# Optimization experiments

Hardware: AMD Instinct MI355X
Metric: run time of the kernel (lower is better)

Reference implementation:

```python
import jax, jax.numpy as jnp
import numpy as np

B, S, E, H = 2, 2048, 1024, 16
D = E // H  # head dim = 64


def setup_inputs() -> dict:
    key = jax.random.key(0)
    ks = jax.random.split(key, 6)
    x = jax.random.normal(ks[0], (B, S, E), dtype=jnp.float32)
    attn_mask = jax.random.bernoulli(ks[1], 0.1, (B, S, S))  # True = masked
    scale = 1.0 / np.sqrt(E)
    w_kernel = jax.random.normal(ks[2], (E, 3 * E), dtype=jnp.float32) * scale
    w_bias = jax.random.normal(ks[3], (3 * E,), dtype=jnp.float32) * 0.02
    fc_kernel = jax.random.normal(ks[4], (E, E), dtype=jnp.float32) * scale
    fc_bias = jax.random.normal(ks[5], (E,), dtype=jnp.float32) * 0.02
    return {"x": x, "attn_mask": attn_mask, "w_kernel": w_kernel,
            "w_bias": w_bias, "fc_kernel": fc_kernel, "fc_bias": fc_bias}


def reference(x, attn_mask, w_kernel, w_bias, fc_kernel, fc_bias):
    b, s, e = x.shape
    qkv = jnp.einsum("bse,ef->bsf", x, w_kernel) + w_bias  # (B,S,3E)
    q, k, v = jnp.split(qkv, 3, axis=-1)

    def heads(t):  # (B,S,E) -> (B,H,S,D)
        return t.reshape(b, s, H, D).transpose(0, 2, 1, 3)

    q, k, v = heads(q), heads(k), heads(v)
    scores = jnp.einsum("bhqd,bhkd->bhqk", q, k) / jnp.sqrt(jnp.float32(D))
    # faithful quirk: masked positions are filled with 1e-9, not -inf
    scores = jnp.where(attn_mask[:, None, :, :], jnp.float32(1e-9), scores)
    A = jax.nn.softmax(scores, axis=-1)
    out = jnp.einsum("bhqk,bhkd->bhqd", A, v)  # (B,H,S,D)
    out = out.transpose(0, 2, 1, 3).reshape(b, s, e)
    # dropout is identity in eval mode
    return jnp.einsum("bse,ef->bsf", out, fc_kernel) + fc_bias
```

## Files before the change

kernel.cpp:

```cpp
#include <hip/hip_runtime.h>
#include <math.h>

#define BB 2
#define SS 2048
#define EE 1024
#define HH 16

typedef _Float16 f16;
typedef __attribute__((ext_vector_type(8))) _Float16 f16x8;
typedef __attribute__((ext_vector_type(4))) _Float16 f16x4;
typedef __attribute__((ext_vector_type(2))) _Float16 f16x2;
typedef __attribute__((ext_vector_type(4))) float f32x4;

union P8 { f16x8 v8; f16x2 h2[4]; };
union V8 { f16x8 v8; f16x4 v4[2]; };

#define QSCALE 0.18033688011112042f

#if __has_builtin(__builtin_amdgcn_exp2f)
#define EXP2(x) __builtin_amdgcn_exp2f(x)
#else
#define EXP2(x) exp2f(x)
#endif

static __device__ __forceinline__ f16x2 pk2(float a, float b) {
#if __has_builtin(__builtin_amdgcn_cvt_pkrtz)
  return __builtin_bit_cast(f16x2, __builtin_amdgcn_cvt_pkrtz(a, b));
#else
  f16x2 r; r[0] = (f16)a; r[1] = (f16)b; return r;
#endif
}

static __device__ __forceinline__ void gl16(const void* g, void* l) {
  __builtin_amdgcn_global_load_lds(
      (const __attribute__((address_space(1))) void*)g,
      (__attribute__((address_space(3))) void*)l, 16, 0, 0);
}

__global__ __launch_bounds__(256) void cvt_f32_f16(
    const float* __restrict__ in, f16* __restrict__ out, int n)
{
  int i = (blockIdx.x * 256 + threadIdx.x) * 8;
  if (i >= n) return;
  float4 a = *(const float4*)(in + i);
  float4 b = *(const float4*)(in + i + 4);
  f16x8 o;
  o[0] = (f16)a.x; o[1] = (f16)a.y; o[2] = (f16)a.z; o[3] = (f16)a.w;
  o[4] = (f16)b.x; o[5] = (f16)b.y; o[6] = (f16)b.z; o[7] = (f16)b.w;
  *(f16x8*)(out + i) = o;
}

__global__ __launch_bounds__(256) void transpose_cvt(
    const float* __restrict__ in, f16* __restrict__ out, int K, int N)
{
  __shared__ float T[64][65];
  const int k0 = blockIdx.y * 64, n0 = blockIdx.x * 64;
  const int tr = threadIdx.x >> 4, tc = (threadIdx.x & 15) * 4;
#pragma unroll
  for (int i = 0; i < 4; ++i) {
    int r = tr + i * 16;
    *(float4*)&T[r][tc] = *(const float4*)(in + (size_t)(k0 + r) * N + n0 + tc);
  }
  __syncthreads();
#pragma unroll
  for (int i = 0; i < 4; ++i) {
    int nl = tr + i * 16;
    f16x4 v;
    v[0] = (f16)T[tc + 0][nl];
    v[1] = (f16)T[tc + 1][nl];
    v[2] = (f16)T[tc + 2][nl];
    v[3] = (f16)T[tc + 3][nl];
    *(f16x4*)(out + (size_t)(n0 + nl) * K + k0 + tc) = v;
  }
}

__global__ __launch_bounds__(256) void pack_mask(
    const int* __restrict__ m, unsigned long long* __restrict__ bits)
{
  const int i = blockIdx.x * 256 + threadIdx.x;
  const unsigned long long bal = __ballot(m[i] != 0);
  if ((threadIdx.x & 63) == 0) bits[i >> 6] = bal;
}

__global__ __launch_bounds__(256) void gemm_f16(
    const f16* __restrict__ A, const f16* __restrict__ Bt,
    const float* __restrict__ bias, int M, int N, int K, int mode,
    f16* __restrict__ oQK, f16* __restrict__ oVT, float* __restrict__ oF32)
{
  __shared__ f16 Ah[128 * 32];
  __shared__ f16 Bh[128 * 32];

  const int t = threadIdx.x;
  const int l = t & 63, w = t >> 6;
  const int l15 = l & 15, l4 = l >> 4;
  const int wr = w >> 1, wc = w & 1;
  const int n0 = blockIdx.x * 128, m0 = blockIdx.y * 128;

  const int srow = l >> 2;
  const int gch  = (l & 3) ^ (srow & 3);
  const f16* Ap0 = A + (size_t)(m0 + w * 32 + srow) * K + gch * 8;
  const f16* Ap1 = Ap0 + (size_t)16 * K;
  const f16* Bp0 = Bt + (size_t)(n0 + w * 32 + srow) * K + gch * 8;
  const f16* Bp1 = Bp0 + (size_t)16 * K;
  f16* ldsA0 = &Ah[(w * 32) * 32];
  f16* ldsA1 = &Ah[(w * 32 + 16) * 32];
  f16* ldsB0 = &Bh[(w * 32) * 32];
  f16* ldsB1 = &Bh[(w * 32 + 16) * 32];

  f32x4 acc[4][4] = {};
  const int csw = (l15 & 3);

  for (int k0 = 0; k0 < K; k0 += 32) {
    gl16(Ap0 + k0, ldsA0);
    gl16(Ap1 + k0, ldsA1);
    gl16(Bp0 + k0, ldsB0);
    gl16(Bp1 + k0, ldsB1);
    __syncthreads();

    f16x8 af[4], bf[4];
#pragma unroll
    for (int mr = 0; mr < 4; ++mr) {
      const int row = wr * 64 + mr * 16 + l15;
      af[mr] = *(const f16x8*)&Ah[row * 32 + ((l4 ^ csw) * 8)];
    }
#pragma unroll
    for (int nr = 0; nr < 4; ++nr) {
      const int row = wc * 64 + nr * 16 + l15;
      bf[nr] = *(const f16x8*)&Bh[row * 32 + ((l4 ^ csw) * 8)];
    }
#pragma unroll
    for (int mr = 0; mr < 4; ++mr)
#pragma unroll
      for (int nr = 0; nr < 4; ++nr)
        acc[mr][nr] = __builtin_amdgcn_mfma_f32_16x16x32_f16(
            af[mr], bf[nr], acc[mr][nr], 0, 0, 0);
    __syncthreads();
  }

  if (mode == 1) {
#pragma unroll
    for (int nr = 0; nr < 4; ++nr) {
      const int n = n0 + wc * 64 + nr * 16 + l15;
      const float bv = bias[n];
#pragma unroll
      for (int mr = 0; mr < 4; ++mr)
#pragma unroll
        for (int j = 0; j < 4; ++j) {
          const int m = m0 + wr * 64 + mr * 16 + l4 * 4 + j;
          oF32[(size_t)m * N + n] = acc[mr][nr][j] + bv;
        }
    }
  } else {
#pragma unroll
    for (int nr = 0; nr < 4; ++nr) {
      const int n = n0 + wc * 64 + nr * 16 + l15;
      const float bv = bias[n];
      if (n < 2048) {
        const float qs = (n < 1024) ? QSCALE : 1.0f;
#pragma unroll
        for (int mr = 0; mr < 4; ++mr)
#pragma unroll
          for (int j = 0; j < 4; ++j) {
            const int m = m0 + wr * 64 + mr * 16 + l4 * 4 + j;
            oQK[(size_t)m * 2048 + n] = (f16)((acc[mr][nr][j] + bv) * qs);
          }
      } else {
        const int hh = (n - 2048) >> 6;
        const int d = (n - 2048) & 63;
#pragma unroll
        for (int mr = 0; mr < 4; ++mr) {
          const int tok0 = m0 + wr * 64 + mr * 16 + l4 * 4;
          const int bq = tok0 >> 11, sq = tok0 & 2047;
          f16x4 v;
          v[0] = (f16)(acc[mr][nr][0] + bv);
          v[1] = (f16)(acc[mr][nr][1] + bv);
          v[2] = (f16)(acc[mr][nr][2] + bv);
          v[3] = (f16)(acc[mr][nr][3] + bv);
          *(f16x4*)(oVT + ((size_t)(bq * 16 + hh) * 64 + d) * SS + sq) = v;
        }
      }
    }
  }
}

__global__ __launch_bounds__(256, 2) void attn_mfma(
    const f16* __restrict__ qkbuf, const f16* __restrict__ vT,
    const unsigned long long* __restrict__ mbits, f16* __restrict__ aout)
{
  __shared__ f16 Kds[2][64 * 64];
  __shared__ f16 Vds[2][64 * 64];

  const int t = threadIdx.x;
  const int w = t >> 6, l = t & 63, l15 = l & 15, l4 = l >> 4;
  const int bh = blockIdx.y, b = bh >> 4, h = bh & 15;
  const int qbase = blockIdx.x * 128 + w * 32;

  f16x8 q00, q01, q10, q11;
  {
    const size_t r0 = (size_t)(b * SS + qbase + l15) * 2048 + h * 64;
    const size_t r1 = (size_t)(b * SS + qbase + 16 + l15) * 2048 + h * 64;
    q00 = *(const f16x8*)(qkbuf + r0 + l4 * 8);
    q01 = *(const f16x8*)(qkbuf + r0 + 32 + l4 * 8);
    q10 = *(const f16x8*)(qkbuf + r1 + l4 * 8);
    q11 = *(const f16x8*)(qkbuf + r1 + 32 + l4 * 8);
  }

  f32x4 accA[4] = {}, accB[4] = {};
  f32x4 accLA = {}, accLB = {};
  f16x8 ones;
#pragma unroll
  for (int i = 0; i < 8; ++i) ones[i] = (f16)1.0f;

  const unsigned long long* mA = mbits + (size_t)(b * SS + qbase + l15) * 32;
  const unsigned long long* mB = mbits + (size_t)(b * SS + qbase + 16 + l15) * 32;

  const int srow = t >> 3;
  const int scb  = (t & 7) * 8;
  const int sws  = (srow & 7) << 3;
  const f16* kb = qkbuf + (size_t)b * SS * 2048 + 1024 + h * 64 + scb;
  const f16* vb = vT + ((size_t)bh * 64 + srow) * SS + scb;

  f16x8 kr0, kr1, vr0, vr1;
#define LOADT(kt)                                                         \
  {                                                                       \
    kr0 = *(const f16x8*)(kb + (size_t)((kt) + srow) * 2048);             \
    kr1 = *(const f16x8*)(kb + (size_t)((kt) + srow + 32) * 2048);        \
    vr0 = *(const f16x8*)(vb + (kt));                                     \
    vr1 = *(const f16x8*)(vb + 32 * SS + (kt));                           \
  }
#define COMMIT(bi)                                                        \
  {                                                                       \
    *(f16x8*)&Kds[bi][srow * 64 + (scb ^ sws)]        = kr0;              \
    *(f16x8*)&Kds[bi][(srow + 32) * 64 + (scb ^ sws)] = kr1;              \
    *(f16x8*)&Vds[bi][srow * 64 + (scb ^ sws)]        = vr0;              \
    *(f16x8*)&Vds[bi][(srow + 32) * 64 + (scb ^ sws)] = vr1;              \
  }

  LOADT(0)
  COMMIT(0)
  LOADT(64)
  __syncthreads();

  const int swr = (l15 & 7) << 3;

  unsigned long long mbA = mA[0], mbB = mB[0];

  for (int tI = 0; tI < 32; ++tI) {
    const int cur = tI & 1;
    unsigned long long nmbA = 0, nmbB = 0;
    if (tI + 1 < 32) { nmbA = mA[tI + 1]; nmbB = mB[tI + 1]; }

#pragma unroll
    for (int sg = 0; sg < 2; ++sg) {
      float pA[8], pB[8];
#pragma unroll
      for (int gh = 0; gh < 2; ++gh) {
        const int g = sg * 2 + gh;
        const f16* krow = &Kds[cur][(g * 16 + l15) * 64];
        const f16x8 k0 = *(const f16x8*)(krow + ((l4 * 8) ^ swr));
        const f16x8 k1 = *(const f16x8*)(krow + ((32 + l4 * 8) ^ swr));
        f32x4 SA = __builtin_amdgcn_mfma_f32_16x16x32_f16(
            k0, q00, (f32x4){0.f, 0.f, 0.f, 0.f}, 0, 0, 0);
        SA = __builtin_amdgcn_mfma_f32_16x16x32_f16(k1, q01, SA, 0, 0, 0);
        f32x4 SB = __builtin_amdgcn_mfma_f32_16x16x32_f16(
            k0, q10, (f32x4){0.f, 0.f, 0.f, 0.f}, 0, 0, 0);
        SB = __builtin_amdgcn_mfma_f32_16x16x32_f16(k1, q11, SB, 0, 0, 0);

        const unsigned int nibA = (unsigned int)(mbA >> (g * 16 + l4 * 4));
        const unsigned int nibB = (unsigned int)(mbB >> (g * 16 + l4 * 4));
#pragma unroll
        for (int j = 0; j < 4; ++j) {
          pA[gh * 4 + j] = ((nibA >> j) & 1u) ? 1.0f : EXP2(SA[j]);
          pB[gh * 4 + j] = ((nibB >> j) & 1u) ? 1.0f : EXP2(SB[j]);
        }
      }
      P8 uA, uB;
      uA.h2[0] = pk2(pA[0], pA[1]); uA.h2[1] = pk2(pA[2], pA[3]);
      uA.h2[2] = pk2(pA[4], pA[5]); uA.h2[3] = pk2(pA[6], pA[7]);
      uB.h2[0] = pk2(pB[0], pB[1]); uB.h2[1] = pk2(pB[2], pB[3]);
      uB.h2[2] = pk2(pB[4], pB[5]); uB.h2[3] = pk2(pB[6], pB[7]);

#pragma unroll
      for (int dg = 0; dg < 4; ++dg) {
        const f16* vrow = &Vds[cur][(dg * 16 + l15) * 64];
        V8 uv;
        uv.v4[0] = *(const f16x4*)(vrow + ((sg * 32 + l4 * 4) ^ swr));
        uv.v4[1] = *(const f16x4*)(vrow + ((sg * 32 + 16 + l4 * 4) ^ swr));
        accA[dg] = __builtin_amdgcn_mfma_f32_16x16x32_f16(uA.v8, uv.v8, accA[dg], 0, 0, 0);
        accB[dg] = __builtin_amdgcn_mfma_f32_16x16x32_f16(uB.v8, uv.v8, accB[dg], 0, 0, 0);
      }
      accLA = __builtin_amdgcn_mfma_f32_16x16x32_f16(uA.v8, ones, accLA, 0, 0, 0);
      accLB = __builtin_amdgcn_mfma_f32_16x16x32_f16(uB.v8, ones, accLB, 0, 0, 0);
    }

    if (tI + 1 < 32) {
      COMMIT(cur ^ 1)
      if (tI + 2 < 32) LOADT((tI + 2) * 64)
    }
    __syncthreads();
    mbA = nmbA; mbB = nmbB;
  }

#pragma unroll
  for (int j = 0; j < 4; ++j) {
    const int qr = l4 * 4 + j;
    const float invA = 1.0f / accLA[j];
    const float invB = 1.0f / accLB[j];
    const size_t rowA = (size_t)(b * SS + qbase + qr) * EE + h * 64 + l15;
    const size_t rowB = (size_t)(b * SS + qbase + 16 + qr) * EE + h * 64 + l15;
#pragma unroll
    for (int dg = 0; dg < 4; ++dg) {
      aout[rowA + dg * 16] = (f16)(accA[dg][j] * invA);
      aout[rowB + dg * 16] = (f16)(accB[dg][j] * invB);
    }
  }
}

extern "C" void kernel_launch(void* const* d_in, const int* in_sizes, int n_in,
                              void* d_out, int out_size, void* d_ws,
                              size_t ws_size, hipStream_t stream)
{
  (void)in_sizes; (void)n_in; (void)out_size; (void)ws_size;
  const float* x   = (const float*)d_in[0];
  const int* mask  = (const int*)d_in[1];
  const float* wk  = (const float*)d_in[2];
  const float* wb  = (const float*)d_in[3];
  const float* fck = (const float*)d_in[4];
  const float* fcb = (const float*)d_in[5];
  float* out       = (float*)d_out;

  char* ws = (char*)d_ws;
  size_t off = 0;
  f16* xh    = (f16*)(ws + off); off += (size_t)4096 * 1024 * 2;
  f16* Wt    = (f16*)(ws + off); off += (size_t)3072 * 1024 * 2;
  f16* fckT  = (f16*)(ws + off); off += (size_t)1024 * 1024 * 2;
  f16* qk    = (f16*)(ws + off); off += (size_t)4096 * 2048 * 2;
  f16* vT    = (f16*)(ws + off); off += (size_t)BB * HH * 64 * SS * 2;
  f16* aoutH = (f16*)(ws + off); off += (size_t)4096 * 1024 * 2;
  unsigned long long* mbits = (unsigned long long*)(ws + off);
  off += (size_t)BB * SS * SS / 8;

  cvt_f32_f16<<<4096 * 1024 / (8 * 256), 256, 0, stream>>>(x, xh, 4096 * 1024);
  transpose_cvt<<<dim3(3072 / 64, 1024 / 64), 256, 0, stream>>>(wk, Wt, 1024, 3072);
  transpose_cvt<<<dim3(1024 / 64, 1024 / 64), 256, 0, stream>>>(fck, fckT, 1024, 1024);
  pack_mask<<<BB * SS * SS / 256, 256, 0, stream>>>(mask, mbits);

  gemm_f16<<<dim3(3072 / 128, 4096 / 128), 256, 0, stream>>>(
      xh, Wt, wb, 4096, 3072, 1024, 0, qk, vT, nullptr);

  attn_mfma<<<dim3(SS / 128, BB * HH), 256, 0, stream>>>(qk, vT, mbits, aoutH);

  gemm_f16<<<dim3(1024 / 128, 4096 / 128), 256, 0, stream>>>(
      aoutH, fckT, fcb, 4096, 1024, 1024, 1, nullptr, nullptr, out);
}
```

Measured before the change: 240.2 us.

## Split attention over two key halves, combine partials; add MFMA priority hints

The attention kernel gains a third grid dimension that splits the 2048 keys into two halves. Each block writes unnormalized fp16 partial outputs plus row sums, and a new combine kernel adds the two halves and normalizes them. The aim is twice as many blocks, for better CU occupancy and latency hiding. In exchange it adds a combine pass, extra global traffic for the partials, and fp16 rounding of the unnormalized partial sums. The change also wraps MFMA sections in s_setprio in both the GEMM and attention kernels, manually unrolls the tile loop by two, and reuses workspace memory for the partial buffers.

After: 253.6 us. 1.06x slower.

```diff
diff --git a/kernel.cpp b/kernel.cpp
--- a/kernel.cpp
+++ b/kernel.cpp
@@ -128,12 +128,14 @@
       const int row = wc * 64 + nr * 16 + l15;
       bf[nr] = *(const f16x8*)&Bh[row * 32 + ((l4 ^ csw) * 8)];
     }
+    __builtin_amdgcn_s_setprio(1);
 #pragma unroll
     for (int mr = 0; mr < 4; ++mr)
 #pragma unroll
       for (int nr = 0; nr < 4; ++nr)
         acc[mr][nr] = __builtin_amdgcn_mfma_f32_16x16x32_f16(
             af[mr], bf[nr], acc[mr][nr], 0, 0, 0);
+    __builtin_amdgcn_s_setprio(0);
     __syncthreads();
   }
 
@@ -185,7 +187,8 @@
 
 __global__ __launch_bounds__(256, 2) void attn_mfma(
     const f16* __restrict__ qkbuf, const f16* __restrict__ vT,
-    const unsigned long long* __restrict__ mbits, f16* __restrict__ aout)
+    const unsigned long long* __restrict__ mbits,
+    f16* __restrict__ Opart, float* __restrict__ Lpart)
 {
   __shared__ f16 Kds[2][64 * 64];
   __shared__ f16 Vds[2][64 * 64];
@@ -193,6 +196,7 @@
   const int t = threadIdx.x;
   const int w = t >> 6, l = t & 63, l15 = l & 15, l4 = l >> 4;
   const int bh = blockIdx.y, b = bh >> 4, h = bh & 15;
+  const int ks = blockIdx.z;
   const int qbase = blockIdx.x * 128 + w * 32;
 
   f16x8 q00, q01, q10, q11;
@@ -211,14 +215,17 @@
 #pragma unroll
   for (int i = 0; i < 8; ++i) ones[i] = (f16)1.0f;
 
-  const unsigned long long* mA = mbits + (size_t)(b * SS + qbase + l15) * 32;
-  const unsigned long long* mB = mbits + (size_t)(b * SS + qbase + 16 + l15) * 32;
+  const unsigned long long* mA =
+      mbits + (size_t)(b * SS + qbase + l15) * 32 + ks * 16;
+  const unsigned long long* mB =
+      mbits + (size_t)(b * SS + qbase + 16 + l15) * 32 + ks * 16;
 
   const int srow = t >> 3;
   const int scb  = (t & 7) * 8;
   const int sws  = (srow & 7) << 3;
-  const f16* kb = qkbuf + (size_t)b * SS * 2048 + 1024 + h * 64 + scb;
-  const f16* vb = vT + ((size_t)bh * 64 + srow) * SS + scb;
+  const f16* kb = qkbuf + (size_t)b * SS * 2048 + 1024 + h * 64 + scb +
+                  (size_t)ks * 1024 * 2048;
+  const f16* vb = vT + ((size_t)bh * 64 + srow) * SS + scb + ks * 1024;
 
   f16x8 kr0, kr1, vr0, vr1;
 #define LOADT(kt)                                                         \
@@ -243,77 +250,107 @@
 
   const int swr = (l15 & 7) << 3;
 
-  unsigned long long mbA = mA[0], mbB = mB[0];
-
-  for (int tI = 0; tI < 32; ++tI) {
-    const int cur = tI & 1;
-    unsigned long long nmbA = 0, nmbB = 0;
-    if (tI + 1 < 32) { nmbA = mA[tI + 1]; nmbB = mB[tI + 1]; }
-
-#pragma unroll
-    for (int sg = 0; sg < 2; ++sg) {
-      float pA[8], pB[8];
-#pragma unroll
-      for (int gh = 0; gh < 2; ++gh) {
-        const int g = sg * 2 + gh;
-        const f16* krow = &Kds[cur][(g * 16 + l15) * 64];
-        const f16x8 k0 = *(const f16x8*)(krow + ((l4 * 8) ^ swr));
-        const f16x8 k1 = *(const f16x8*)(krow + ((32 + l4 * 8) ^ swr));
-        f32x4 SA = __builtin_amdgcn_mfma_f32_16x16x32_f16(
-            k0, q00, (f32x4){0.f, 0.f, 0.f, 0.f}, 0, 0, 0);
-        SA = __builtin_amdgcn_mfma_f32_16x16x32_f16(k1, q01, SA, 0, 0, 0);
-        f32x4 SB = __builtin_amdgcn_mfma_f32_16x16x32_f16(
-            k0, q10, (f32x4){0.f, 0.f, 0.f, 0.f}, 0, 0, 0);
-        SB = __builtin_amdgcn_mfma_f32_16x16x32_f16(k1, q11, SB, 0, 0, 0);
-
-        const unsigned int nibA = (unsigned int)(mbA >> (g * 16 + l4 * 4));
-        const unsigned int nibB = (unsigned int)(mbB >> (g * 16 + l4 * 4));
-#pragma unroll
-        for (int j = 0; j < 4; ++j) {
-          pA[gh * 4 + j] = ((nibA >> j) & 1u) ? 1.0f : EXP2(SA[j]);
-          pB[gh * 4 + j] = ((nibB >> j) & 1u) ? 1.0f : EXP2(SB[j]);
-        }
-      }
-      P8 uA, uB;
-      uA.h2[0] = pk2(pA[0], pA[1]); uA.h2[1] = pk2(pA[2], pA[3]);
-      uA.h2[2] = pk2(pA[4], pA[5]); uA.h2[3] = pk2(pA[6], pA[7]);
-      uB.h2[0] = pk2(pB[0], pB[1]); uB.h2[1] = pk2(pB[2], pB[3]);
-      uB.h2[2] = pk2(pB[4], pB[5]); uB.h2[3] = pk2(pB[6], pB[7]);
-
-#pragma unroll
-      for (int dg = 0; dg < 4; ++dg) {
-        const f16* vrow = &Vds[cur][(dg * 16 + l15) * 64];
-        V8 uv;
-        uv.v4[0] = *(const f16x4*)(vrow + ((sg * 32 + l4 * 4) ^ swr));
-        uv.v4[1] = *(const f16x4*)(vrow + ((sg * 32 + 16 + l4 * 4) ^ swr));
-        accA[dg] = __builtin_amdgcn_mfma_f32_16x16x32_f16(uA.v8, uv.v8, accA[dg], 0, 0, 0);
-        accB[dg] = __builtin_amdgcn_mfma_f32_16x16x32_f16(uB.v8, uv.v8, accB[dg], 0, 0, 0);
-      }
-      accLA = __builtin_amdgcn_mfma_f32_16x16x32_f16(uA.v8, ones, accLA, 0, 0, 0);
-      accLB = __builtin_amdgcn_mfma_f32_16x16x32_f16(uB.v8, ones, accLB, 0, 0, 0);
-    }
-
-    if (tI + 1 < 32) {
-      COMMIT(cur ^ 1)
-      if (tI + 2 < 32) LOADT((tI + 2) * 64)
-    }
-    __syncthreads();
-    mbA = nmbA; mbB = nmbB;
-  }
-
+#define BODY(cur, tI)                                                         \
+  {                                                                           \
+    const unsigned long long mbA = mA[tI];                                    \
+    const unsigned long long mbB = mB[tI];                                    \
+    _Pragma("unroll")                                                         \
+    for (int sg = 0; sg < 2; ++sg) {                                          \
+      float pA[8], pB[8];                                                     \
+      _Pragma("unroll")                                                       \
+      for (int gh = 0; gh < 2; ++gh) {                                        \
+        const int g = sg * 2 + gh;                                            \
+        const f16* krow = &Kds[cur][(g * 16 + l15) * 64];                     \
+        const f16x8 k0 = *(const f16x8*)(krow + ((l4 * 8) ^ swr));            \
+        const f16x8 k1 = *(const f16x8*)(krow + ((32 + l4 * 8) ^ swr));       \
+        __builtin_amdgcn_s_setprio(1);                                        \
+        f32x4 SA = __builtin_amdgcn_mfma_f32_16x16x32_f16(                    \
+            k0, q00, (f32x4){0.f, 0.f, 0.f, 0.f}, 0, 0, 0);                   \
+        SA = __builtin_amdgcn_mfma_f32_16x16x32_f16(k1, q01, SA, 0, 0, 0);    \
+        f32x4 SB = __builtin_amdgcn_mfma_f32_16x16x32_f16(                    \
+            k0, q10, (f32x4){0.f, 0.f, 0.f, 0.f}, 0, 0, 0);                   \
+        SB = __builtin_amdgcn_mfma_f32_16x16x32_f16(k1, q11, SB, 0, 0, 0);    \
+        __builtin_amdgcn_s_setprio(0);                                        \
+        const unsigned int nibA = (unsigned int)(mbA >> (g * 16 + l4 * 4));   \
+        const unsigned int nibB = (unsigned int)(mbB >> (g * 16 + l4 * 4));   \
+        _Pragma("unroll")                                                     \
+        for (int j = 0; j < 4; ++j) {                                         \
+          pA[gh * 4 + j] = ((nibA >> j) & 1u) ? 1.0f : EXP2(SA[j]);           \
+          pB[gh * 4 + j] = ((nibB >> j) & 1u) ? 1.0f : EXP2(SB[j]);           \
+        }                                                                     \
+      }                                                                       \
+      P8 uA, uB;                                                              \
+      uA.h2[0] = pk2(pA[0], pA[1]); uA.h2[1] = pk2(pA[2], pA[3]);             \
+      uA.h2[2] = pk2(pA[4], pA[5]); uA.h2[3] = pk2(pA[6], pA[7]);             \
+      uB.h2[0] = pk2(pB[0], pB[1]); uB.h2[1] = pk2(pB[2], pB[3]);             \
+      uB.h2[2] = pk2(pB[4], pB[5]); uB.h2[3] = pk2(pB[6], pB[7]);             \
+      __builtin_amdgcn_s_setprio(1);                                          \
+      _Pragma("unroll")                                                       \
+      for (int dg = 0; dg < 4; ++dg) {                                        \
+        const f16* vrow = &Vds[cur][(dg * 16 + l15) * 64];                    \
+        V8 uv;                                                                \
+        uv.v4[0] = *(const f16x4*)(vrow + ((sg * 32 + l4 * 4) ^ swr));        \
+        uv.v4[1] = *(const f16x4*)(vrow + ((sg * 32 + 16 + l4 * 4) ^ swr));   \
+        accA[dg] = __builtin_amdgcn_mfma_f32_16x16x32_f16(uA.v8, uv.v8,       \
+                                                          accA[dg], 0, 0, 0); \
+        accB[dg] = __builtin_amdgcn_mfma_f32_16x16x32_f16(uB.v8, uv.v8,       \
+                                                          accB[dg], 0, 0, 0); \
+      }                                                                       \
+      accLA = __builtin_amdgcn_mfma_f32_16x16x32_f16(uA.v8, ones, accLA,      \
+                                                     0, 0, 0);                \
+      accLB = __builtin_amdgcn_mfma_f32_16x16x32_f16(uB.v8, ones, accLB,      \
+                                                     0, 0, 0);                \
+      __builtin_amdgcn_s_setprio(0);                                          \
+    }                                                                         \
+    if ((tI) + 1 < 16) {                                                      \
+      COMMIT((cur) ^ 1)                                                       \
+      if ((tI) + 2 < 16) LOADT(((tI) + 2) * 64)                               \
+    }                                                                         \
+    __syncthreads();                                                          \
+  }
+
+  for (int tI = 0; tI < 16; tI += 2) {
+    BODY(0, tI)
+    BODY(1, tI + 1)
+  }
+
+  const size_t obase = (size_t)ks * 4096 * EE;
 #pragma unroll
   for (int j = 0; j < 4; ++j) {
     const int qr = l4 * 4 + j;
-    const float invA = 1.0f / accLA[j];
-    const float invB = 1.0f / accLB[j];
     const size_t rowA = (size_t)(b * SS + qbase + qr) * EE + h * 64 + l15;
     const size_t rowB = (size_t)(b * SS + qbase + 16 + qr) * EE + h * 64 + l15;
 #pragma unroll
     for (int dg = 0; dg < 4; ++dg) {
-      aout[rowA + dg * 16] = (f16)(accA[dg][j] * invA);
-      aout[rowB + dg * 16] = (f16)(accB[dg][j] * invB);
-    }
-  }
+      Opart[obase + rowA + dg * 16] = (f16)accA[dg][j];
+      Opart[obase + rowB + dg * 16] = (f16)accB[dg][j];
+    }
+    if (l15 == 0) {
+      Lpart[(size_t)ks * 4096 * HH + (size_t)(b * SS + qbase + qr) * HH + h] =
+          accLA[j];
+      Lpart[(size_t)ks * 4096 * HH +
+            (size_t)(b * SS + qbase + 16 + qr) * HH + h] = accLB[j];
+    }
+  }
+}
+
+__global__ __launch_bounds__(256) void combine(
+    const f16* __restrict__ Opart, const float* __restrict__ Lpart,
+    f16* __restrict__ aout)
+{
+  const size_t i = ((size_t)blockIdx.x * 256 + threadIdx.x) * 8;
+  const int token = (int)(i >> 10);
+  const int h = (int)((i >> 6) & 15);
+  const float inv =
+      1.0f / (Lpart[(size_t)token * HH + h] +
+              Lpart[(size_t)4096 * HH + (size_t)token * HH + h]);
+  const f16x8 o0 = *(const f16x8*)(Opart + i);
+  const f16x8 o1 = *(const f16x8*)(Opart + (size_t)4096 * EE + i);
+  f16x8 o;
+#pragma unroll
+  for (int j = 0; j < 8; ++j)
+    o[j] = (f16)(((float)o0[j] + (float)o1[j]) * inv);
+  *(f16x8*)(aout + i) = o;
 }
 
 extern "C" void kernel_launch(void* const* d_in, const int* in_sizes, int n_in,
@@ -330,15 +367,16 @@
   float* out       = (float*)d_out;
 
   char* ws = (char*)d_ws;
-  size_t off = 0;
-  f16* xh    = (f16*)(ws + off); off += (size_t)4096 * 1024 * 2;
-  f16* Wt    = (f16*)(ws + off); off += (size_t)3072 * 1024 * 2;
-  f16* fckT  = (f16*)(ws + off); off += (size_t)1024 * 1024 * 2;
-  f16* qk    = (f16*)(ws + off); off += (size_t)4096 * 2048 * 2;
-  f16* vT    = (f16*)(ws + off); off += (size_t)BB * HH * 64 * SS * 2;
-  f16* aoutH = (f16*)(ws + off); off += (size_t)4096 * 1024 * 2;
-  unsigned long long* mbits = (unsigned long long*)(ws + off);
-  off += (size_t)BB * SS * SS / 8;
+  f16* fckT = (f16*)(ws);
+  f16* qk   = (f16*)(ws + 2097152);
+  f16* vT   = (f16*)(ws + 18874368);
+  unsigned long long* mbits = (unsigned long long*)(ws + 27262976);
+  float* Lp = (float*)(ws + 28311552);
+  char* scratch = ws + 28835840;
+  f16* xh    = (f16*)scratch;
+  f16* Wt    = (f16*)(scratch + 8388608);
+  f16* Opart = (f16*)scratch;
+  f16* aoutH = qk;
 
   cvt_f32_f16<<<4096 * 1024 / (8 * 256), 256, 0, stream>>>(x, xh, 4096 * 1024);
   transpose_cvt<<<dim3(3072 / 64, 1024 / 64), 256, 0, stream>>>(wk, Wt, 1024, 3072);
@@ -348,7 +386,9 @@
   gemm_f16<<<dim3(3072 / 128, 4096 / 128), 256, 0, stream>>>(
       xh, Wt, wb, 4096, 3072, 1024, 0, qk, vT, nullptr);
 
-  attn_mfma<<<dim3(SS / 128, BB * HH), 256, 0, stream>>>(qk, vT, mbits, aoutH);
+  attn_mfma<<<dim3(SS / 128, BB * HH, 2), 256, 0, stream>>>(
+      qk, vT, mbits, Opart, Lp);
+  combine<<<4096 * 1024 / (8 * 256), 256, 0, stream>>>(Opart, Lp, aoutH);
 
   gemm_f16<<<dim3(1024 / 128, 4096 / 128), 256, 0, stream>>>(
       aoutH, fckT, fcb, 4096, 1024, 1024, 1, nullptr, nullptr, out);
```
